# Performance work log

Hardware: AMD Instinct MI355X
Metric: run time of the kernel (lower is better)

Reference implementation:

```python
import jax, jax.numpy as jnp
import numpy as np

RADIUS = 0.1
NSAMPLE = 32


def ball_query(xyz, new_xyz, radius, nsample):
    """xyz:(B,N,3), new_xyz:(B,P,3) -> idx:(B,P,nsample) int32.
    Semantics of PointNet++ CUDA ball_query: first `nsample` points (in index
    order) within `radius`; remaining slots padded with the first found index
    (0 if no point is within radius)."""
    d2 = jnp.sum((new_xyz[:, :, None, :] - xyz[:, None, :, :]) ** 2, axis=-1)  # (B,P,N)
    mask = d2 < radius * radius
    cnt = jnp.cumsum(mask, axis=-1) - 1               # rank of each hit
    valid = mask & (cnt < nsample)
    first = jnp.argmax(mask, axis=-1)                 # first in-ball index (0 if none)
    B, P, N = d2.shape
    pos = jnp.where(valid, cnt, nsample)              # invalid -> dump slot
    buf = jnp.broadcast_to(first[..., None], (B, P, nsample + 1))
    j = jnp.broadcast_to(jnp.arange(N)[None, None, :], (B, P, N))
    b = jnp.arange(B)[:, None, None]
    p = jnp.arange(P)[None, :, None]
    buf = buf.at[b, p, pos].set(j)
    return buf[..., :nsample].astype(jnp.int32)


def setup_inputs() -> dict:
    key = jax.random.key(0)
    k1, k2, k3 = jax.random.split(key, 3)
    xyz = jax.random.uniform(k1, (2, 16384, 3), dtype=jnp.float32)
    new_xyz = jax.random.uniform(k2, (2, 4096, 3), dtype=jnp.float32)
    features = jax.random.normal(k3, (2, 64, 16384), dtype=jnp.float32)
    return {"xyz": xyz, "new_xyz": new_xyz, "features": features}


def reference(xyz, new_xyz, features):
    idx = ball_query(xyz, new_xyz, RADIUS, NSAMPLE)              # (B,P,S)
    grouped_xyz = jax.vmap(lambda x, i: x[i])(xyz, idx)          # (B,P,S,3)
    grouped_xyz = jnp.transpose(grouped_xyz, (0, 3, 1, 2))       # (B,3,P,S)
    grouped_xyz = grouped_xyz - jnp.transpose(new_xyz, (0, 2, 1))[..., None]
    grouped_feat = jax.vmap(lambda f, i: f[:, i])(features, idx) # (B,C,P,S)
    return jnp.concatenate([grouped_xyz, grouped_feat], axis=1)  # (B,3+C,P,S)
```

## Files before the change

kernel.cpp:

```cpp
#include <hip/hip_runtime.h>
#include <hip/hip_bf16.h>
#include <climits>

#define BATCH   2
#define NPTS    16384
#define NQ      4096
#define CFEAT   64
#define NS      32
#define R2      0.01f
#define COUT    (3 + CFEAT)
#define GDIM    10
#define NCELL   (GDIM * GDIM * GDIM)
#define NWORDS  (NPTS / 32)

#define FEATT_BYTES ((size_t)BATCH * NPTS * CFEAT * sizeof(unsigned short))
#define PXYZJ_BYTES ((size_t)BATCH * NPTS * sizeof(float4))
#define OFF_CNT    0
#define OFF_FILL   (2 * NCELL)
#define OFF_CSTART (4 * NCELL)
#define GRID_INTS  (4 * NCELL + 2 * (NCELL + 1))

__device__ __forceinline__ int cell_of(float x, float y, float z) {
    int cx = (int)(x * GDIM); cx = cx < 0 ? 0 : (cx > GDIM - 1 ? GDIM - 1 : cx);
    int cy = (int)(y * GDIM); cy = cy < 0 ? 0 : (cy > GDIM - 1 ? GDIM - 1 : cy);
    int cz = (int)(z * GDIM); cz = cz < 0 ? 0 : (cz > GDIM - 1 ? GDIM - 1 : cz);
    return (cz * GDIM + cy) * GDIM + cx;
}

__device__ __forceinline__ unsigned short f2bf(float f) {
    unsigned b = __float_as_uint(f);
    return (unsigned short)((b + 0x7FFFu + ((b >> 16) & 1u)) >> 16);
}

__device__ __forceinline__ void st_nt(float* p, float v) {
    __builtin_nontemporal_store(v, p);
}

__global__ __launch_bounds__(256) void prep1_kernel(
    const float* __restrict__ feat, unsigned short* __restrict__ featT16,
    const float* __restrict__ xyz, int* __restrict__ cnt)
{
    __shared__ float tile[64][65];
    if (blockIdx.x < 512) {
        const int b    = blockIdx.x >> 8;
        const int n0   = (blockIdx.x & 255) * 64;
        const int lane = threadIdx.x & 63;
        const int grp  = threadIdx.x >> 6;
        const float* fb = feat + (size_t)b * CFEAT * NPTS;
        #pragma unroll
        for (int k = 0; k < 16; ++k) {
            const int c = grp * 16 + k;
            tile[c][lane] = fb[(size_t)c * NPTS + n0 + lane];
        }
        __syncthreads();
        unsigned short* db = featT16 + ((size_t)b * NPTS + n0) * CFEAT;
        #pragma unroll
        for (int k = 0; k < 8; ++k) {
            const int e   = threadIdx.x + 256 * k;
            const int row = e >> 5;
            const int c2  = e & 31;
            ushort2 v;
            v.x = f2bf(tile[2 * c2][row]);
            v.y = f2bf(tile[2 * c2 + 1][row]);
            ((ushort2*)(db + (size_t)row * CFEAT))[c2] = v;
        }
    } else {
        const int g = (blockIdx.x - 512) * 256 + threadIdx.x;
        const int b = g >> 14;
        const int c = cell_of(xyz[g*3], xyz[g*3+1], xyz[g*3+2]);
        atomicAdd(&cnt[b * NCELL + c], 1);
    }
}

__global__ __launch_bounds__(256) void prep2_kernel(
    const float* __restrict__ xyz, const int* __restrict__ cnt,
    int* __restrict__ fill, int* __restrict__ cstart,
    float4* __restrict__ pxyzj)
{
    __shared__ int scs[2 * NCELL];
    const int tid  = threadIdx.x;
    const int lane = tid & 63;

    if (tid < 128) {
        const int b = tid >> 6;
        int c16[16];
        int tot = 0;
        #pragma unroll
        for (int k = 0; k < 16; ++k) {
            const int i = lane * 16 + k;
            c16[k] = (i < NCELL) ? cnt[b * NCELL + i] : 0;
            tot += c16[k];
        }
        int ex = tot;
        #pragma unroll
        for (int off = 1; off < 64; off <<= 1) {
            const int u = __shfl_up(ex, off);
            if (lane >= off) ex += u;
        }
        ex -= tot;
        int run = ex;
        #pragma unroll
        for (int k = 0; k < 16; ++k) {
            const int i = lane * 16 + k;
            if (i < NCELL) scs[b * NCELL + i] = run;
            run += c16[k];
        }
    }
    __syncthreads();

    if (blockIdx.x == 0) {
        for (int i = tid; i < 2 * (NCELL + 1); i += 256) {
            const int b  = i / (NCELL + 1);
            const int ci = i - b * (NCELL + 1);
            cstart[i] = (ci == NCELL) ? NPTS : scs[b * NCELL + ci];
        }
    }

    const int g = blockIdx.x * 256 + tid;
    const int b = g >> 14;
    const int j = g & (NPTS - 1);
    const float x = xyz[g*3], y = xyz[g*3+1], z = xyz[g*3+2];
    const int c = cell_of(x, y, z);
    const int pos = atomicAdd(&fill[b * NCELL + c], 1);
    pxyzj[b * NPTS + scs[b * NCELL + c] + pos] =
        make_float4(x, y, z, __int_as_float(j));
}

__global__ __launch_bounds__(256, 8) void qg_fused(
    const float* __restrict__ xyz,
    const float* __restrict__ new_xyz,
    const int* __restrict__ cstart,
    const float4* __restrict__ pxyzj,
    const unsigned short* __restrict__ featT16,
    float* __restrict__ out)
{
    const int tid  = threadIdx.x;
    const int wave = tid >> 6;
    const int lane = tid & 63;
    const int q    = (blockIdx.x << 2) + wave;
    const int b    = q >> 12;
    const int p    = q & (NQ - 1);

    __shared__ __align__(16) unsigned char smem[4 * 2176];
    unsigned char* wbase = smem + wave * 2176;
    unsigned int* hmask  = (unsigned int*)wbase;
    int* idx_s           = (int*)(wbase + 2048);

    {
        uint4 z; z.x = 0; z.y = 0; z.z = 0; z.w = 0;
        ((uint4*)hmask)[lane * 2]     = z;
        ((uint4*)hmask)[lane * 2 + 1] = z;
    }

    const float qx = new_xyz[q * 3 + 0];
    const float qy = new_xyz[q * 3 + 1];
    const float qz = new_xyz[q * 3 + 2];
    const float* xb = xyz + (size_t)b * NPTS * 3;
    const int* cs = cstart + b * (NCELL + 1);
    const float4* pb = pxyzj + (size_t)b * NPTS;

    int qcx = (int)(qx * GDIM); qcx = qcx < 0 ? 0 : (qcx > GDIM-1 ? GDIM-1 : qcx);
    int qcy = (int)(qy * GDIM); qcy = qcy < 0 ? 0 : (qcy > GDIM-1 ? GDIM-1 : qcy);
    int qcz = (int)(qz * GDIM); qcz = qcz < 0 ? 0 : (qcz > GDIM-1 ? GDIM-1 : qcz);
    const int x0 = qcx > 0 ? qcx - 1 : 0;
    const int x1 = qcx < GDIM-1 ? qcx + 1 : GDIM-1;
    const int y0 = qcy > 0 ? qcy - 1 : 0;
    const int y1 = qcy < GDIM-1 ? qcy + 1 : GDIM-1;
    const int z0 = qcz > 0 ? qcz - 1 : 0;
    const int z1 = qcz < GDIM-1 ? qcz + 1 : GDIM-1;
    const int ny  = y1 - y0 + 1;
    const int nyz = ny * (z1 - z0 + 1);

    int sv = 0, ev = 0;
    if (lane < nyz) {
        const int gzi = (ny == 3) ? ((lane * 86) >> 8) : (lane >> 1);
        const int gyi = lane - gzi * ny;
        const int crow = ((z0 + gzi) * GDIM + (y0 + gyi)) * GDIM;
        sv = cs[crow + x0];
        ev = cs[crow + x1 + 1];
    }
    __builtin_amdgcn_wave_barrier();

    {
        int len = (lane < nyz) ? (ev - sv) : 0;
        int pfx = len;
        #pragma unroll
        for (int off = 1; off < 16; off <<= 1) {
            const int u = __shfl_up(pfx, off);
            if (lane >= off) pfx += u;
        }
        const int T  = __builtin_amdgcn_readfirstlane(__shfl(pfx, 15));
        const int pe = pfx - len;

        const int b0 = __builtin_amdgcn_readfirstlane(__shfl(sv, 0));
        const int p1 = __builtin_amdgcn_readfirstlane(__shfl(pe, 1));
        const int b1 = __builtin_amdgcn_readfirstlane(__shfl(sv, 1)) - p1;
        const int p2 = __builtin_amdgcn_readfirstlane(__shfl(pe, 2));
        const int b2 = __builtin_amdgcn_readfirstlane(__shfl(sv, 2)) - p2;
        const int p3 = __builtin_amdgcn_readfirstlane(__shfl(pe, 3));
        const int b3 = __builtin_amdgcn_readfirstlane(__shfl(sv, 3)) - p3;
        const int p4 = __builtin_amdgcn_readfirstlane(__shfl(pe, 4));
        const int b4 = __builtin_amdgcn_readfirstlane(__shfl(sv, 4)) - p4;
        const int p5 = __builtin_amdgcn_readfirstlane(__shfl(pe, 5));
        const int b5 = __builtin_amdgcn_readfirstlane(__shfl(sv, 5)) - p5;
        const int p6 = __builtin_amdgcn_readfirstlane(__shfl(pe, 6));
        const int b6 = __builtin_amdgcn_readfirstlane(__shfl(sv, 6)) - p6;
        const int p7 = __builtin_amdgcn_readfirstlane(__shfl(pe, 7));
        const int b7 = __builtin_amdgcn_readfirstlane(__shfl(sv, 7)) - p7;
        const int p8 = __builtin_amdgcn_readfirstlane(__shfl(pe, 8));
        const int b8 = __builtin_amdgcn_readfirstlane(__shfl(sv, 8)) - p8;

        for (int t0 = 0; t0 < T; t0 += 64) {
            const int t = t0 + lane;
            int bsel = b0;
            bsel = (t >= p1) ? b1 : bsel;
            bsel = (t >= p2) ? b2 : bsel;
            bsel = (t >= p3) ? b3 : bsel;
            bsel = (t >= p4) ? b4 : bsel;
            bsel = (t >= p5) ? b5 : bsel;
            bsel = (t >= p6) ? b6 : bsel;
            bsel = (t >= p7) ? b7 : bsel;
            bsel = (t >= p8) ? b8 : bsel;
            const bool valid = t < T;
            const int i = valid ? (bsel + t) : 0;
            const float4 pt = pb[i];
            const float dx = pt.x - qx;
            const float dy = pt.y - qy;
            const float dz = pt.z - qz;
            if (valid && (dx*dx + dy*dy + dz*dz < R2)) {
                const int j = __float_as_int(pt.w);
                atomicOr(&hmask[j >> 5], 1u << (j & 31));
            }
        }
    }
    __builtin_amdgcn_wave_barrier();

    int K;
    {
        unsigned int w[8];
        const uint4 a = ((const uint4*)hmask)[lane * 2];
        const uint4 c = ((const uint4*)hmask)[lane * 2 + 1];
        w[0] = a.x; w[1] = a.y; w[2] = a.z; w[3] = a.w;
        w[4] = c.x; w[5] = c.y; w[6] = c.z; w[7] = c.w;

        int cnt8 = 0;
        #pragma unroll
        for (int k = 0; k < 8; ++k) cnt8 += __popc(w[k]);

        int pfx = cnt8;
        #pragma unroll
        for (int off = 1; off < 64; off <<= 1) {
            const int u = __shfl_up(pfx, off);
            if (lane >= off) pfx += u;
        }
        K = __shfl(pfx, 63);
        pfx -= cnt8;

        if (pfx < NS && cnt8 > 0) {
            int r = pfx;
            #pragma unroll
            for (int k = 0; k < 8; ++k) {
                unsigned int m = w[k];
                while (m && r < NS) {
                    const int bit = __builtin_ctz(m);
                    idx_s[r] = lane * 256 + k * 32 + bit;
                    m &= m - 1;
                    ++r;
                }
            }
        }
        __builtin_amdgcn_wave_barrier();
        if (lane < NS && lane >= K) {
            idx_s[lane] = (K > 0) ? idx_s[0] : 0;
        }
        __builtin_amdgcn_wave_barrier();
    }

    const int sm = lane >> 1;
    const int h  = lane & 1;
    const int jrow = idx_s[sm];
    const unsigned short* base16 = featT16 +
        ((size_t)b * NPTS + jrow) * CFEAT + (h << 5);

    const size_t cstride = (size_t)NQ * NS;
    const size_t out_q   = ((size_t)b * COUT * NQ + (size_t)p) * NS;

    float xv = 0.f, yv = 0.f, zv = 0.f;
    if (lane < NS) {
        const int j = idx_s[lane];
        xv = xb[j*3+0] - qx;
        yv = xb[j*3+1] - qy;
        zv = xb[j*3+2] - qz;
    }

    const uint4 ga = ((const uint4*)base16)[0];
    const uint4 gb = ((const uint4*)base16)[1];

    if (lane < NS) {
        st_nt(&out[out_q + 0*cstride + lane], xv);
        st_nt(&out[out_q + 1*cstride + lane], yv);
        st_nt(&out[out_q + 2*cstride + lane], zv);
    }

    float* fob = out + out_q + (size_t)(3 + (h << 5)) * cstride + sm;
    #define ST2(kk, u) \
        st_nt(&fob[(size_t)(2*(kk))     * cstride], __uint_as_float((u) << 16)); \
        st_nt(&fob[(size_t)(2*(kk) + 1) * cstride], __uint_as_float((u) & 0xFFFF0000u))

    ST2(0, ga.x); ST2(1, ga.y); ST2(2, ga.z); ST2(3, ga.w);
    ST2(4, gb.x); ST2(5, gb.y); ST2(6, gb.z); ST2(7, gb.w);

    const uint4 gc = ((const uint4*)base16)[2];
    const uint4 gd = ((const uint4*)base16)[3];

    ST2(8,  gc.x); ST2(9,  gc.y); ST2(10, gc.z); ST2(11, gc.w);
    ST2(12, gd.x); ST2(13, gd.y); ST2(14, gd.z); ST2(15, gd.w);
    #undef ST2
}

__global__ __launch_bounds__(256) void qg_linear(
    const float* __restrict__ xyz, const float* __restrict__ new_xyz,
    const float* __restrict__ feat, float* __restrict__ out)
{
    const int wave = threadIdx.x >> 6;
    const int lane = threadIdx.x & 63;
    const int bp   = blockIdx.x * 4 + wave;
    const int b    = bp >> 12;
    const int p    = bp & (NQ - 1);
    __shared__ int idx_s[4][NS];
    const float qx = new_xyz[bp*3+0], qy = new_xyz[bp*3+1], qz = new_xyz[bp*3+2];
    const float* xb = xyz + (size_t)b * NPTS * 3;
    int cnt = 0;
    const unsigned long long below = (1ull << lane) - 1ull;
    for (int base = 0; base < NPTS; base += 64) {
        const int j = base + lane;
        const float dx = xb[j*3+0]-qx, dy = xb[j*3+1]-qy, dz = xb[j*3+2]-qz;
        const bool hit = dx*dx+dy*dy+dz*dz < R2;
        const unsigned long long m = __ballot(hit);
        if (hit) {
            const int slot = cnt + __popcll(m & below);
            if (slot < NS) idx_s[wave][slot] = j;
        }
        cnt += __popcll(m);
        if (cnt >= NS) break;
    }
    __builtin_amdgcn_wave_barrier();
    if (cnt < NS) {
        const int first = (cnt > 0) ? idx_s[wave][0] : 0;
        if (lane >= cnt && lane < NS) idx_s[wave][lane] = first;
    }
    __builtin_amdgcn_wave_barrier();
    const size_t cstride = (size_t)NQ * NS;
    const size_t out_q = ((size_t)b * COUT * NQ + (size_t)p) * NS;
    if (lane < NS) {
        const int j = idx_s[wave][lane];
        out[out_q + 0*cstride + lane] = xb[j*3+0] - qx;
        out[out_q + 1*cstride + lane] = xb[j*3+1] - qy;
        out[out_q + 2*cstride + lane] = xb[j*3+2] - qz;
    }
    const float* fb = feat + (size_t)b * CFEAT * NPTS;
    const int s = lane & 31, half = lane >> 5;
    const int j = idx_s[wave][s];
    #pragma unroll 8
    for (int c = half; c < CFEAT; c += 2)
        out[out_q + (size_t)(3 + c) * cstride + s] = fb[(size_t)c * NPTS + j];
}

extern "C" void kernel_launch(void* const* d_in, const int* in_sizes, int n_in,
                              void* d_out, int out_size, void* d_ws, size_t ws_size,
                              hipStream_t stream) {
    const float* xyz     = (const float*)d_in[0];
    const float* new_xyz = (const float*)d_in[1];
    const float* feat    = (const float*)d_in[2];
    float* out = (float*)d_out;

    const size_t need_full = FEATT_BYTES + PXYZJ_BYTES + (size_t)GRID_INTS * sizeof(int);

    if (ws_size >= need_full) {
        unsigned short* featT16 = (unsigned short*)d_ws;
        float4* pxyzj = (float4*)((char*)d_ws + FEATT_BYTES);
        int* gi = (int*)((char*)d_ws + FEATT_BYTES + PXYZJ_BYTES);
        int* cnt    = gi + OFF_CNT;
        int* fill   = gi + OFF_FILL;
        int* cstart = gi + OFF_CSTART;

        hipMemsetAsync(cnt, 0, 4 * NCELL * sizeof(int), stream);
        prep1_kernel<<<512 + (BATCH * NPTS) / 256, 256, 0, stream>>>(feat, featT16, xyz, cnt);
        prep2_kernel<<<(BATCH * NPTS) / 256, 256, 0, stream>>>(xyz, cnt, fill, cstart, pxyzj);
        qg_fused<<<(BATCH * NQ) / 4, 256, 0, stream>>>(
            xyz, new_xyz, cstart, pxyzj, featT16, out);
    } else {
        qg_linear<<<(BATCH * NQ) / 4, 256, 0, stream>>>(xyz, new_xyz, feat, out);
    }
}
```

Before: 115.3 us.

## Fuse grid build and feature transpose into one prep kernel with shared-memory histogram

```diff
diff --git a/kernel.cpp b/kernel.cpp
--- a/kernel.cpp
+++ b/kernel.cpp
@@ -15,10 +15,8 @@
 
 #define FEATT_BYTES ((size_t)BATCH * NPTS * CFEAT * sizeof(unsigned short))
 #define PXYZJ_BYTES ((size_t)BATCH * NPTS * sizeof(float4))
-#define OFF_CNT    0
-#define OFF_FILL   (2 * NCELL)
-#define OFF_CSTART (4 * NCELL)
-#define GRID_INTS  (4 * NCELL + 2 * (NCELL + 1))
+#define OFF_CSTART 0
+#define GRID_INTS  (2 * (NCELL + 1))
 
 __device__ __forceinline__ int cell_of(float x, float y, float z) {
     int cx = (int)(x * GDIM); cx = cx < 0 ? 0 : (cx > GDIM - 1 ? GDIM - 1 : cx);
@@ -36,16 +34,75 @@
     __builtin_nontemporal_store(v, p);
 }
 
-__global__ __launch_bounds__(256) void prep1_kernel(
+__global__ __launch_bounds__(256) void prep_all(
     const float* __restrict__ feat, unsigned short* __restrict__ featT16,
-    const float* __restrict__ xyz, int* __restrict__ cnt)
+    const float* __restrict__ xyz, int* __restrict__ cstart,
+    float4* __restrict__ pxyzj)
 {
-    __shared__ float tile[64][65];
-    if (blockIdx.x < 512) {
-        const int b    = blockIdx.x >> 8;
-        const int n0   = (blockIdx.x & 255) * 64;
-        const int lane = threadIdx.x & 63;
-        const int grp  = threadIdx.x >> 6;
+    __shared__ __align__(16) unsigned char smem[64 * 65 * sizeof(float)];
+    const int tid = threadIdx.x;
+
+    if (blockIdx.x < 2) {
+        const int b = blockIdx.x;
+        int* hist   = (int*)smem;
+        int* starts = (int*)smem + NCELL;
+
+        for (int i = tid; i < NCELL; i += 256) hist[i] = 0;
+        __syncthreads();
+
+        const float* xb = xyz + (size_t)b * NPTS * 3;
+        for (int i = tid; i < NPTS; i += 256) {
+            const int c = cell_of(xb[i*3], xb[i*3+1], xb[i*3+2]);
+            atomicAdd(&hist[c], 1);
+        }
+        __syncthreads();
+
+        if (tid < 64) {
+            const int lane = tid;
+            int c16[16];
+            int tot = 0;
+            #pragma unroll
+            for (int k = 0; k < 16; ++k) {
+                const int i = lane * 16 + k;
+                c16[k] = (i < NCELL) ? hist[i] : 0;
+                tot += c16[k];
+            }
+            int ex = tot;
+            #pragma unroll
+            for (int off = 1; off < 64; off <<= 1) {
+                const int u = __shfl_up(ex, off);
+                if (lane >= off) ex += u;
+            }
+            ex -= tot;
+            int run = ex;
+            #pragma unroll
+            for (int k = 0; k < 16; ++k) {
+                const int i = lane * 16 + k;
+                if (i < NCELL) starts[i] = run;
+                run += c16[k];
+            }
+        }
+        __syncthreads();
+
+        int* csb = cstart + b * (NCELL + 1);
+        for (int i = tid; i <= NCELL; i += 256)
+            csb[i] = (i == NCELL) ? NPTS : starts[i];
+        __syncthreads();
+
+        float4* pbb = pxyzj + (size_t)b * NPTS;
+        for (int i = tid; i < NPTS; i += 256) {
+            const float x = xb[i*3], y = xb[i*3+1], z = xb[i*3+2];
+            const int c = cell_of(x, y, z);
+            const int pos = atomicAdd(&starts[c], 1);
+            pbb[pos] = make_float4(x, y, z, __int_as_float(i));
+        }
+    } else {
+        float (*tile)[65] = (float(*)[65])smem;
+        const int t    = blockIdx.x - 2;
+        const int b    = t >> 8;
+        const int n0   = (t & 255) * 64;
+        const int lane = tid & 63;
+        const int grp  = tid >> 6;
         const float* fb = feat + (size_t)b * CFEAT * NPTS;
         #pragma unroll
         for (int k = 0; k < 16; ++k) {
@@ -56,7 +113,7 @@
         unsigned short* db = featT16 + ((size_t)b * NPTS + n0) * CFEAT;
         #pragma unroll
         for (int k = 0; k < 8; ++k) {
-            const int e   = threadIdx.x + 256 * k;
+            const int e   = tid + 256 * k;
             const int row = e >> 5;
             const int c2  = e & 31;
             ushort2 v;
@@ -64,66 +121,7 @@
             v.y = f2bf(tile[2 * c2 + 1][row]);
             ((ushort2*)(db + (size_t)row * CFEAT))[c2] = v;
         }
-    } else {
-        const int g = (blockIdx.x - 512) * 256 + threadIdx.x;
-        const int b = g >> 14;
-        const int c = cell_of(xyz[g*3], xyz[g*3+1], xyz[g*3+2]);
-        atomicAdd(&cnt[b * NCELL + c], 1);
-    }
-}
-
-__global__ __launch_bounds__(256) void prep2_kernel(
-    const float* __restrict__ xyz, const int* __restrict__ cnt,
-    int* __restrict__ fill, int* __restrict__ cstart,
-    float4* __restrict__ pxyzj)
-{
-    __shared__ int scs[2 * NCELL];
-    const int tid  = threadIdx.x;
-    const int lane = tid & 63;
-
-    if (tid < 128) {
-        const int b = tid >> 6;
-        int c16[16];
-        int tot = 0;
-        #pragma unroll
-        for (int k = 0; k < 16; ++k) {
-            const int i = lane * 16 + k;
-            c16[k] = (i < NCELL) ? cnt[b * NCELL + i] : 0;
-            tot += c16[k];
-        }
-        int ex = tot;
-        #pragma unroll
-        for (int off = 1; off < 64; off <<= 1) {
-            const int u = __shfl_up(ex, off);
-            if (lane >= off) ex += u;
-        }
-        ex -= tot;
-        int run = ex;
-        #pragma unroll
-        for (int k = 0; k < 16; ++k) {
-            const int i = lane * 16 + k;
-            if (i < NCELL) scs[b * NCELL + i] = run;
-            run += c16[k];
-        }
-    }
-    __syncthreads();
-
-    if (blockIdx.x == 0) {
-        for (int i = tid; i < 2 * (NCELL + 1); i += 256) {
-            const int b  = i / (NCELL + 1);
-            const int ci = i - b * (NCELL + 1);
-            cstart[i] = (ci == NCELL) ? NPTS : scs[b * NCELL + ci];
-        }
-    }
-
-    const int g = blockIdx.x * 256 + tid;
-    const int b = g >> 14;
-    const int j = g & (NPTS - 1);
-    const float x = xyz[g*3], y = xyz[g*3+1], z = xyz[g*3+2];
-    const int c = cell_of(x, y, z);
-    const int pos = atomicAdd(&fill[b * NCELL + c], 1);
-    pxyzj[b * NPTS + scs[b * NCELL + c] + pos] =
-        make_float4(x, y, z, __int_as_float(j));
+    }
 }
 
 __global__ __launch_bounds__(256, 8) void qg_fused(
@@ -379,14 +377,9 @@
     if (ws_size >= need_full) {
         unsigned short* featT16 = (unsigned short*)d_ws;
         float4* pxyzj = (float4*)((char*)d_ws + FEATT_BYTES);
-        int* gi = (int*)((char*)d_ws + FEATT_BYTES + PXYZJ_BYTES);
-        int* cnt    = gi + OFF_CNT;
-        int* fill   = gi + OFF_FILL;
-        int* cstart = gi + OFF_CSTART;
-
-        hipMemsetAsync(cnt, 0, 4 * NCELL * sizeof(int), stream);
-        prep1_kernel<<<512 + (BATCH * NPTS) / 256, 256, 0, stream>>>(feat, featT16, xyz, cnt);
-        prep2_kernel<<<(BATCH * NPTS) / 256, 256, 0, stream>>>(xyz, cnt, fill, cstart, pxyzj);
+        int* cstart = (int*)((char*)d_ws + FEATT_BYTES + PXYZJ_BYTES);
+
+        prep_all<<<2 + 512, 256, 0, stream>>>(feat, featT16, xyz, cstart, pxyzj);
         qg_fused<<<(BATCH * NQ) / 4, 256, 0, stream>>>(
             xyz, new_xyz, cstart, pxyzj, featT16, out);
     } else {
```

After: 150.8 us. 30.8% more time.
